# Kernel optimization log

Hardware: AMD Instinct MI355X
Metric: run time of the kernel (lower is better)

## Reference

```python
import jax, jax.numpy as jnp
import numpy as np

# Static model configuration (matches init_kwargs)
Hh, Ww = 48, 48
L = Hh * Ww            # 2304 flattened lattice sites
NH, HD = 8, 32         # heads, head_dim
D = NH * HD            # d_model = 256
MLP = 1024
NL = 4                 # num transformer blocks
RADIUS = 2             # local attention window radius
MAXD = 7               # relative position clipping
NB = 2 * MAXD + 1      # bias buckets per axis = 15
EPS = 1e-6
B = 4


def _coords():
    ys = jnp.arange(Hh)
    xs = jnp.arange(Ww)
    yy, xx = jnp.meshgrid(ys, xs, indexing='ij')
    return jnp.stack([yy, xx], axis=-1).reshape(L, 2)  # (L,2) int


def _local_mask():
    c = _coords()
    dy = jnp.abs(c[:, None, 0] - c[None, :, 0])
    dx = jnp.abs(c[:, None, 1] - c[None, :, 1])
    dy = jnp.minimum(dy, Hh - dy)  # periodic (torus)
    dx = jnp.minimum(dx, Ww - dx)
    allowed = (dy <= RADIUS) & (dx <= RADIUS)
    return jnp.where(allowed, 0.0, -1e9).astype(jnp.float32)  # (L,L)


def _rel_bias(rel_emb):
    c = _coords()
    dy = c[:, None, 0] - c[None, :, 0]
    dx = c[:, None, 1] - c[None, :, 1]
    # shortest signed periodic differences
    dy = (dy + Hh // 2) % Hh - Hh // 2
    dx = (dx + Ww // 2) % Ww - Ww // 2
    dyb = (jnp.clip(dy, -MAXD, MAXD) + MAXD).astype(jnp.int32)
    dxb = (jnp.clip(dx, -MAXD, MAXD) + MAXD).astype(jnp.int32)
    return rel_emb[:, dyb, dxb]  # (NH, L, L)


def _ln(x, s, b):
    mu = jnp.mean(x, axis=-1, keepdims=True)
    var = jnp.var(x, axis=-1, keepdims=True)
    return (x - mu) * jax.lax.rsqrt(var + EPS) * s + b


def setup_inputs() -> dict:
    key = jax.random.key(0)
    ks = jax.random.split(key, 16)
    sc = 0.05
    inp = {
        'x': jax.random.randint(ks[0], (B, Hh, Ww), 0, 2, dtype=jnp.int32),
        'Win': jax.random.normal(ks[1], (3, D), jnp.float32) * sc,
        'b_in': jnp.zeros((D,), jnp.float32),
        'lnA_s': jnp.ones((NL, D), jnp.float32),
        'lnA_b': jnp.zeros((NL, D), jnp.float32),
        'Wq': jax.random.normal(ks[2], (NL, D, NH, HD), jnp.float32) * sc,
        'bq': jnp.zeros((NL, NH, HD), jnp.float32),
        'Wk': jax.random.normal(ks[3], (NL, D, NH, HD), jnp.float32) * sc,
        'bk': jnp.zeros((NL, NH, HD), jnp.float32),
        'Wv': jax.random.normal(ks[4], (NL, D, NH, HD), jnp.float32) * sc,
        'bv': jnp.zeros((NL, NH, HD), jnp.float32),
        'Wo': jax.random.normal(ks[5], (NL, NH, HD, D), jnp.float32) * sc,
        'bo': jnp.zeros((NL, D), jnp.float32),
        'lnB_s': jnp.ones((NL, D), jnp.float32),
        'lnB_b': jnp.zeros((NL, D), jnp.float32),
        'W1': jax.random.normal(ks[6], (NL, D, MLP), jnp.float32) * sc,
        'b1': jnp.zeros((NL, MLP), jnp.float32),
        'W2': jax.random.normal(ks[7], (NL, MLP, D), jnp.float32) * sc,
        'b2': jnp.zeros((NL, D), jnp.float32),
        'rel_emb': jax.random.normal(ks[8], (NH, NB, NB), jnp.float32) * 0.02,
        'lnF_s': jnp.ones((D,), jnp.float32),
        'lnF_b': jnp.zeros((D,), jnp.float32),
        'Wout': jax.random.normal(ks[9], (D, 1), jnp.float32) * sc,
        'bout': jnp.zeros((1,), jnp.float32),
    }
    return inp


def reference(x, Win, b_in, lnA_s, lnA_b, Wq, bq, Wk, bk, Wv, bv, Wo, bo,
              lnB_s, lnB_b, W1, b1, W2, b2, rel_emb, lnF_s, lnF_b, Wout, bout):
    xf = x.astype(jnp.float32)[..., None]                     # (B,H,W,1)
    ys = jnp.arange(Hh, dtype=jnp.float32) / max(Hh - 1, 1)
    xs = jnp.arange(Ww, dtype=jnp.float32) / max(Ww - 1, 1)
    yy, xx = jnp.meshgrid(ys, xs, indexing='ij')
    coords = jnp.broadcast_to(jnp.stack([yy, xx], -1), (x.shape[0], Hh, Ww, 2))
    feats = jnp.concatenate([xf, coords], -1).reshape(x.shape[0], L, 3)

    h = feats @ Win + b_in                                    # (B,L,D)

    # combined additive attention bias: local periodic mask + learned 2D rel-pos bias
    cb = _local_mask()[None, None] + _rel_bias(rel_emb)[None]  # (1,NH,L,L)
    scale = 1.0 / np.sqrt(HD).astype(np.float32)

    for i in range(NL):
        y = _ln(h, lnA_s[i], lnA_b[i])
        q = jnp.einsum('bld,dhe->blhe', y, Wq[i]) + bq[i]
        k = jnp.einsum('bld,dhe->blhe', y, Wk[i]) + bk[i]
        v = jnp.einsum('bld,dhe->blhe', y, Wv[i]) + bv[i]
        scores = jnp.einsum('bqhe,bkhe->bhqk', q, k) * scale + cb
        p = jax.nn.softmax(scores, axis=-1)
        att = jnp.einsum('bhqk,bkhe->bqhe', p, v)
        y = jnp.einsum('bqhe,hed->bqd', att, Wo[i]) + bo[i]
        h = h + y
        y = _ln(h, lnB_s[i], lnB_b[i])
        y = jax.nn.gelu(y @ W1[i] + b1[i]) @ W2[i] + b2[i]
        h = h + y

    h = _ln(h, lnF_s, lnF_b)
    logits = (h @ Wout + bout)[..., 0].reshape(x.shape[0], Hh, Ww)
    return logits
```

## Files before the change

kernel.cpp:

```cpp
#include <hip/hip_runtime.h>
#include <hip/hip_bf16.h>
#include <math.h>

#define NT_   9216
#define D_    256
#define NH_   8
#define HD_   32
#define L_    2304
#define HH_   48
#define WW_   48
#define MLP_  1024
#define NL_   4

typedef __attribute__((ext_vector_type(8))) short bf16x8;
typedef __attribute__((ext_vector_type(4))) float f32x4;

__device__ __forceinline__ float gelu_tanh(float x) {
    const float c0 = 0.7978845608028654f;
    const float c1 = 0.044715f;
    float u = c0 * (x + c1 * x * x * x);
    return 0.5f * x * (1.0f + tanhf(u));
}

__device__ __forceinline__ void gload16(const void* gsrc, void* ldst) {
    __builtin_amdgcn_global_load_lds(
        (const __attribute__((address_space(1))) void*)gsrc,
        (__attribute__((address_space(3))) void*)ldst, 16, 0, 0);
}

__device__ __forceinline__ unsigned short f2bf(float f) {
    __hip_bfloat16 h = __float2bfloat16(f);
    return *(unsigned short*)&h;
}

__global__ void tcvt_kernel(const float* __restrict__ in, __hip_bfloat16* __restrict__ out,
                            int K, int N, int inLayerStride, int outLayerStride) {
    __shared__ float t[32][33];
    int l = blockIdx.z;
    int n0 = blockIdx.x * 32, k0 = blockIdx.y * 32;
    int tx = threadIdx.x, ty = threadIdx.y;
    const float* src = in + (size_t)l * inLayerStride;
    #pragma unroll
    for (int r = 0; r < 32; r += 8)
        t[ty + r][tx] = src[(size_t)(k0 + ty + r) * N + n0 + tx];
    __syncthreads();
    __hip_bfloat16* dst = out + (size_t)l * outLayerStride;
    #pragma unroll
    for (int r = 0; r < 32; r += 8)
        dst[(size_t)(n0 + ty + r) * K + k0 + tx] = __float2bfloat16(t[tx][ty + r]);
}

__global__ void bcat_kernel(const float* __restrict__ bq, const float* __restrict__ bk,
                            const float* __restrict__ bv, float* __restrict__ bqkv) {
    int l = blockIdx.x, n = threadIdx.x;
    float v = (n < 256) ? bq[l * 256 + n] : (n < 512 ? bk[l * 256 + n - 256] : bv[l * 256 + n - 512]);
    bqkv[l * 768 + n] = v;
}

__global__ void embed_kernel(const int* __restrict__ x, const float* __restrict__ Win,
                             const float* __restrict__ b_in, float* __restrict__ h) {
    int t = blockIdx.x, d = threadIdx.x;
    int l = t % L_;
    int yy = l / WW_, xx = l % WW_;
    float xv = (float)x[t];
    float yn = yy * (1.0f / 47.0f);
    float xn = xx * (1.0f / 47.0f);
    h[t * D_ + d] = xv * Win[d] + yn * Win[D_ + d] + xn * Win[2 * D_ + d] + b_in[d];
}

__global__ void ln_kernel(const float* __restrict__ h, const float* __restrict__ s,
                          const float* __restrict__ bb, __hip_bfloat16* __restrict__ y) {
    int wid = threadIdx.x >> 6, lane = threadIdx.x & 63;
    int t = (blockIdx.x << 2) + wid;
    float4 v = *(const float4*)(h + (size_t)t * D_ + lane * 4);
    float sum = v.x + v.y + v.z + v.w;
    float sq  = v.x * v.x + v.y * v.y + v.z * v.z + v.w * v.w;
    #pragma unroll
    for (int off = 32; off; off >>= 1) {
        sum += __shfl_xor(sum, off);
        sq  += __shfl_xor(sq,  off);
    }
    float mu  = sum * (1.0f / D_);
    float var = sq * (1.0f / D_) - mu * mu;
    float rs  = rsqrtf(var + 1e-6f);
    float4 s4 = *(const float4*)(s  + lane * 4);
    float4 b4 = *(const float4*)(bb + lane * 4);
    ushort4 o;
    o.x = f2bf((v.x - mu) * rs * s4.x + b4.x);
    o.y = f2bf((v.y - mu) * rs * s4.y + b4.y);
    o.z = f2bf((v.z - mu) * rs * s4.z + b4.z);
    o.w = f2bf((v.w - mu) * rs * s4.w + b4.w);
    *(ushort4*)(y + (size_t)t * D_ + lane * 4) = o;
}

__global__ __launch_bounds__(256)
void attn_kernel(const float* __restrict__ qkv, const float* __restrict__ rel_emb,
                 __hip_bfloat16* __restrict__ att) {
    __shared__ float ks[144 * 36];
    __shared__ float vsd[144 * 36];

    const int tile = blockIdx.x;
    const int hh   = blockIdx.y;
    const int b    = blockIdx.z;
    const int ty   = tile / 6, tx = tile - ty * 6;
    const int y0   = ty * 8,  x0  = tx * 8;
    const int tid  = threadIdx.x;

    for (int idx = tid; idx < 144 * 32; idx += 256) {
        int r = idx >> 5, d = idx & 31;
        int ly = r / 12, lx = r - ly * 12;
        int gy = y0 + ly - 2; gy += (gy < 0) ? HH_ : 0; gy -= (gy >= HH_) ? HH_ : 0;
        int gx = x0 + lx - 2; gx += (gx < 0) ? WW_ : 0; gx -= (gx >= WW_) ? WW_ : 0;
        const float* row = qkv + (size_t)(b * L_ + gy * WW_ + gx) * 768 + hh * HD_;
        ks[r * 36 + d]  = row[256 + d];
        vsd[r * 36 + d] = row[512 + d];
    }
    __syncthreads();

    const int g = tid >> 5;
    const int j = tid & 31;
    const bool valid = (j < 25);
    const int oy2 = j / 5, ox2 = j - oy2 * 5;

    const float bias = rel_emb[hh * 225 + (9 - oy2) * 15 + (9 - ox2)];

    for (int s = 0; s < 8; ++s) {
        const int t = b * L_ + (y0 + g) * WW_ + (x0 + s);

        const float* qp = qkv + (size_t)t * 768 + hh * HD_;
        const int hr = valid ? ((g + oy2) * 12 + (s + ox2)) : 0;
        const float* kp = ks + hr * 36;

        float dot = 0.f;
        #pragma unroll
        for (int d = 0; d < 8; ++d) {
            float4 q4 = ((const float4*)qp)[d];
            float4 k4 = ((const float4*)kp)[d];
            dot += q4.x * k4.x + q4.y * k4.y + q4.z * k4.z + q4.w * k4.w;
        }
        float sc = valid ? (dot * 0.17677669529663687f + bias) : -1e30f;

        float m = sc;
        #pragma unroll
        for (int off = 16; off; off >>= 1) m = fmaxf(m, __shfl_xor(m, off, 32));
        float p = __expf(sc - m);
        float sum = p;
        #pragma unroll
        for (int off = 16; off; off >>= 1) sum += __shfl_xor(sum, off, 32);
        float inv = 1.0f / sum;

        float acc = 0.f;
        #pragma unroll
        for (int n = 0; n < 25; ++n) {
            float pn = __shfl(p, n, 32);
            int   rn = (g + n / 5) * 12 + (s + n % 5);
            acc += pn * vsd[rn * 36 + j];
        }
        att[t * D_ + hh * HD_ + j] = __float2bfloat16(acc * inv);
    }
}

template<int EPI>
__global__ __launch_bounds__(256, 2)
void mgemm(const __hip_bfloat16* __restrict__ A, const __hip_bfloat16* __restrict__ BT,
           const float* __restrict__ bias, const float* res,
           float* Cf, __hip_bfloat16* Cb, int M, int N, int K) {
    __shared__ __hip_bfloat16 As[128 * 32];
    __shared__ __hip_bfloat16 Bs[128 * 32];
    const int bm = blockIdx.y * 128, bn = blockIdx.x * 128;
    const int tid = threadIdx.x, lane = tid & 63, wv = tid >> 6;
    const int wm = (wv >> 1) * 64, wn = (wv & 1) * 64;

    const __hip_bfloat16* aSrc = A + (size_t)(bm + 16 * wv + (lane >> 2)) * K + (lane & 3) * 8;
    const __hip_bfloat16* bSrc = BT + (size_t)(bn + 16 * wv + (lane >> 2)) * K + (lane & 3) * 8;
    __hip_bfloat16* aDst0 = As + wv * 512;
    __hip_bfloat16* aDst1 = As + (wv + 4) * 512;
    __hip_bfloat16* bDst0 = Bs + wv * 512;
    __hip_bfloat16* bDst1 = Bs + (wv + 4) * 512;
    const size_t rowJump = (size_t)64 * K;

    f32x4 acc[4][4];
    #pragma unroll
    for (int i = 0; i < 4; ++i)
        #pragma unroll
        for (int j = 0; j < 4; ++j)
            acc[i][j] = (f32x4){0.f, 0.f, 0.f, 0.f};

    const int rsel = (lane & 15);
    const int ko   = (lane >> 4) * 8;

    for (int k0 = 0; k0 < K; k0 += 32) {
        gload16(aSrc,            aDst0);
        gload16(aSrc + rowJump,  aDst1);
        gload16(bSrc,            bDst0);
        gload16(bSrc + rowJump,  bDst1);
        __syncthreads();

        bf16x8 af[4], bfr[4];
        #pragma unroll
        for (int f = 0; f < 4; ++f) {
            af[f]  = *(const bf16x8*)(As + (wm + f * 16 + rsel) * 32 + ko);
            bfr[f] = *(const bf16x8*)(Bs + (wn + f * 16 + rsel) * 32 + ko);
        }
        #pragma unroll
        for (int i = 0; i < 4; ++i)
            #pragma unroll
            for (int j = 0; j < 4; ++j)
                acc[i][j] = __builtin_amdgcn_mfma_f32_16x16x32_bf16(af[i], bfr[j], acc[i][j], 0, 0, 0);
        __syncthreads();
        aSrc += 32; bSrc += 32;
    }

    #pragma unroll
    for (int i = 0; i < 4; ++i) {
        #pragma unroll
        for (int r = 0; r < 4; ++r) {
            int rr = bm + wm + i * 16 + (lane >> 4) * 4 + r;
            #pragma unroll
            for (int j = 0; j < 4; ++j) {
                int cc = bn + wn + j * 16 + rsel;
                float v = acc[i][j][r] + bias[cc];
                if (EPI == 2) {
                    Cb[(size_t)rr * N + cc] = __float2bfloat16(gelu_tanh(v));
                } else {
                    if (EPI == 1) v += res[(size_t)rr * N + cc];
                    Cf[(size_t)rr * N + cc] = v;
                }
            }
        }
    }
}

__global__ void final_kernel(const float* __restrict__ h, const float* __restrict__ s,
                             const float* __restrict__ bb, const float* __restrict__ Wout,
                             const float* __restrict__ bout, float* __restrict__ out) {
    int t = blockIdx.x, d = threadIdx.x;
    float v = h[t * D_ + d];
    float a = v, b2 = v * v;
    #pragma unroll
    for (int off = 32; off; off >>= 1) {
        a  += __shfl_xor(a,  off);
        b2 += __shfl_xor(b2, off);
    }
    __shared__ float red[8];
    __shared__ float red2[4];
    int wave = threadIdx.x >> 6;
    if ((threadIdx.x & 63) == 0) { red[wave] = a; red[4 + wave] = b2; }
    __syncthreads();
    float sum   = red[0] + red[1] + red[2] + red[3];
    float sumsq = red[4] + red[5] + red[6] + red[7];
    float mu  = sum * (1.0f / D_);
    float var = sumsq * (1.0f / D_) - mu * mu;
    float rs  = rsqrtf(var + 1e-6f);
    float yv  = (v - mu) * rs * s[d] + bb[d];
    float p   = yv * Wout[d];
    #pragma unroll
    for (int off = 32; off; off >>= 1) p += __shfl_xor(p, off);
    if ((threadIdx.x & 63) == 0) red2[wave] = p;
    __syncthreads();
    if (threadIdx.x == 0)
        out[t] = red2[0] + red2[1] + red2[2] + red2[3] + bout[0];
}

extern "C" void kernel_launch(void* const* d_in, const int* in_sizes, int n_in,
                              void* d_out, int out_size, void* d_ws, size_t ws_size,
                              hipStream_t stream) {
    const int*   x       = (const int*)  d_in[0];
    const float* Win     = (const float*)d_in[1];
    const float* b_in    = (const float*)d_in[2];
    const float* lnA_s   = (const float*)d_in[3];
    const float* lnA_b   = (const float*)d_in[4];
    const float* Wq      = (const float*)d_in[5];
    const float* bq      = (const float*)d_in[6];
    const float* Wk      = (const float*)d_in[7];
    const float* bk      = (const float*)d_in[8];
    const float* Wv      = (const float*)d_in[9];
    const float* bv      = (const float*)d_in[10];
    const float* Wo      = (const float*)d_in[11];
    const float* bo      = (const float*)d_in[12];
    const float* lnB_s   = (const float*)d_in[13];
    const float* lnB_b   = (const float*)d_in[14];
    const float* W1      = (const float*)d_in[15];
    const float* b1      = (const float*)d_in[16];
    const float* W2      = (const float*)d_in[17];
    const float* b2      = (const float*)d_in[18];
    const float* rel_emb = (const float*)d_in[19];
    const float* lnF_s   = (const float*)d_in[20];
    const float* lnF_b   = (const float*)d_in[21];
    const float* Wout    = (const float*)d_in[22];
    const float* bout    = (const float*)d_in[23];
    float* out = (float*)d_out;

    float* ws = (float*)d_ws;
    float*          h      = ws;
    __hip_bfloat16* y      = (__hip_bfloat16*)(ws + 2359296);
    float*          qkv    = ws + 3538944;
    __hip_bfloat16* att    = (__hip_bfloat16*)(ws + 10616832);
    __hip_bfloat16* tbuf   = (__hip_bfloat16*)qkv;
    __hip_bfloat16* WqkvT  = (__hip_bfloat16*)(ws + 11796480);
    __hip_bfloat16* WoT    = WqkvT + 4 * 768 * 256;
    __hip_bfloat16* W1T    = WoT   + 4 * 256 * 256;
    __hip_bfloat16* W2T    = W1T   + 4 * 1024 * 256;
    float*          bqkv   = (float*)(W2T + 4 * 256 * 1024);

    dim3 blk(256);
    dim3 tb(32, 8);

    tcvt_kernel<<<dim3(8, 8, 4),  tb, 0, stream>>>(Wq, WqkvT,              256, 256,  65536, 196608);
    tcvt_kernel<<<dim3(8, 8, 4),  tb, 0, stream>>>(Wk, WqkvT + 256 * 256,  256, 256,  65536, 196608);
    tcvt_kernel<<<dim3(8, 8, 4),  tb, 0, stream>>>(Wv, WqkvT + 512 * 256,  256, 256,  65536, 196608);
    tcvt_kernel<<<dim3(8, 8, 4),  tb, 0, stream>>>(Wo, WoT,                256, 256,  65536, 65536);
    tcvt_kernel<<<dim3(32, 8, 4), tb, 0, stream>>>(W1, W1T,                256, 1024, 262144, 262144);
    tcvt_kernel<<<dim3(8, 32, 4), tb, 0, stream>>>(W2, W2T,                1024, 256, 262144, 262144);
    bcat_kernel<<<4, 768, 0, stream>>>(bq, bk, bv, bqkv);

    embed_kernel<<<NT_, blk, 0, stream>>>(x, Win, b_in, h);

    for (int l = 0; l < NL_; ++l) {
        const __hip_bfloat16* wqkv = WqkvT + (size_t)l * 768 * 256;
        const __hip_bfloat16* wo   = WoT   + (size_t)l * 256 * 256;
        const __hip_bfloat16* w1   = W1T   + (size_t)l * 1024 * 256;
        const __hip_bfloat16* w2   = W2T   + (size_t)l * 256 * 1024;

        ln_kernel<<<NT_ / 4, blk, 0, stream>>>(h, lnA_s + l * D_, lnA_b + l * D_, y);

        mgemm<0><<<dim3(6, 72), blk, 0, stream>>>(y, wqkv, bqkv + l * 768, nullptr,
                                                  qkv, nullptr, NT_, 768, 256);
        attn_kernel<<<dim3(36, 8, 4), blk, 0, stream>>>(qkv, rel_emb, att);
        mgemm<1><<<dim3(2, 72), blk, 0, stream>>>(att, wo, bo + l * D_, h,
                                                  h, nullptr, NT_, 256, 256);

        ln_kernel<<<NT_ / 4, blk, 0, stream>>>(h, lnB_s + l * D_, lnB_b + l * D_, y);

        mgemm<2><<<dim3(8, 72), blk, 0, stream>>>(y, w1, b1 + l * MLP_, nullptr,
                                                  nullptr, tbuf, NT_, 1024, 256);
        mgemm<1><<<dim3(2, 72), blk, 0, stream>>>(tbuf, w2, b2 + l * D_, h,
                                                  h, nullptr, NT_, 256, 1024);
    }

    final_kernel<<<NT_, blk, 0, stream>>>(h, lnF_s, lnF_b, Wout, bout, out);
}
```

Before: 666.0 us.

## Fuse weight prep launches, vectorize attention K/V loads, remap GEMM tiles per XCD

Merges the six weight transpose/convert launches and the bias concat into a single prep kernel, removing several kernel launches. The attention kernel now stages K/V halo rows into shared memory with float4 loads instead of scalar loads. The GEMM remaps its linear block index so consecutive tiles are grouped per XCD (stride by 8), aiming for better L2 locality on the multi-die chip. The remap assumes the block count is divisible by 8.

```diff
diff --git a/kernel.cpp b/kernel.cpp
--- a/kernel.cpp
+++ b/kernel.cpp
@@ -33,28 +33,56 @@
     return *(unsigned short*)&h;
 }
 
-__global__ void tcvt_kernel(const float* __restrict__ in, __hip_bfloat16* __restrict__ out,
-                            int K, int N, int inLayerStride, int outLayerStride) {
+__global__ void prep_kernel(const float* __restrict__ Wq, const float* __restrict__ Wk,
+                            const float* __restrict__ Wv, const float* __restrict__ Wo,
+                            const float* __restrict__ W1, const float* __restrict__ W2,
+                            const float* __restrict__ bq, const float* __restrict__ bk,
+                            const float* __restrict__ bv,
+                            __hip_bfloat16* __restrict__ WqkvT, __hip_bfloat16* __restrict__ WoT,
+                            __hip_bfloat16* __restrict__ W1T, __hip_bfloat16* __restrict__ W2T,
+                            float* __restrict__ bqkv) {
+    int bid = blockIdx.x;
+    int tid = threadIdx.y * 32 + threadIdx.x;
+    if (bid >= 3072) {
+        int l = bid - 3072;
+        for (int n = tid; n < 768; n += 256) {
+            float v = (n < 256) ? bq[l * 256 + n]
+                    : (n < 512 ? bk[l * 256 + n - 256] : bv[l * 256 + n - 512]);
+            bqkv[l * 768 + n] = v;
+        }
+        return;
+    }
+    int l = bid / 768, rem = bid - l * 768;
+    const float* src; __hip_bfloat16* dst;
+    int K, N, n0, k0;
+    if (rem < 256) {
+        int which = rem >> 6, tidx = rem & 63;
+        n0 = (tidx & 7) * 32; k0 = (tidx >> 3) * 32;
+        K = 256; N = 256;
+        if (which == 0)      { src = Wq + (size_t)l * 65536; dst = WqkvT + (size_t)l * 196608; }
+        else if (which == 1) { src = Wk + (size_t)l * 65536; dst = WqkvT + (size_t)l * 196608 + 65536; }
+        else if (which == 2) { src = Wv + (size_t)l * 65536; dst = WqkvT + (size_t)l * 196608 + 131072; }
+        else                 { src = Wo + (size_t)l * 65536; dst = WoT   + (size_t)l * 65536; }
+    } else if (rem < 512) {
+        int tidx = rem - 256;
+        n0 = (tidx & 31) * 32; k0 = (tidx >> 5) * 32;
+        K = 256; N = 1024;
+        src = W1 + (size_t)l * 262144; dst = W1T + (size_t)l * 262144;
+    } else {
+        int tidx = rem - 512;
+        n0 = (tidx & 7) * 32; k0 = (tidx >> 3) * 32;
+        K = 1024; N = 256;
+        src = W2 + (size_t)l * 262144; dst = W2T + (size_t)l * 262144;
+    }
     __shared__ float t[32][33];
-    int l = blockIdx.z;
-    int n0 = blockIdx.x * 32, k0 = blockIdx.y * 32;
     int tx = threadIdx.x, ty = threadIdx.y;
-    const float* src = in + (size_t)l * inLayerStride;
     #pragma unroll
     for (int r = 0; r < 32; r += 8)
         t[ty + r][tx] = src[(size_t)(k0 + ty + r) * N + n0 + tx];
     __syncthreads();
-    __hip_bfloat16* dst = out + (size_t)l * outLayerStride;
     #pragma unroll
     for (int r = 0; r < 32; r += 8)
         dst[(size_t)(n0 + ty + r) * K + k0 + tx] = __float2bfloat16(t[tx][ty + r]);
-}
-
-__global__ void bcat_kernel(const float* __restrict__ bq, const float* __restrict__ bk,
-                            const float* __restrict__ bv, float* __restrict__ bqkv) {
-    int l = blockIdx.x, n = threadIdx.x;
-    float v = (n < 256) ? bq[l * 256 + n] : (n < 512 ? bk[l * 256 + n - 256] : bv[l * 256 + n - 512]);
-    bqkv[l * 768 + n] = v;
 }
 
 __global__ void embed_kernel(const int* __restrict__ x, const float* __restrict__ Win,
@@ -106,14 +134,14 @@
     const int y0   = ty * 8,  x0  = tx * 8;
     const int tid  = threadIdx.x;
 
-    for (int idx = tid; idx < 144 * 32; idx += 256) {
-        int r = idx >> 5, d = idx & 31;
+    for (int idx = tid; idx < 144 * 8; idx += 256) {
+        int r = idx >> 3, c = (idx & 7) * 4;
         int ly = r / 12, lx = r - ly * 12;
         int gy = y0 + ly - 2; gy += (gy < 0) ? HH_ : 0; gy -= (gy >= HH_) ? HH_ : 0;
         int gx = x0 + lx - 2; gx += (gx < 0) ? WW_ : 0; gx -= (gx >= WW_) ? WW_ : 0;
-        const float* row = qkv + (size_t)(b * L_ + gy * WW_ + gx) * 768 + hh * HD_;
-        ks[r * 36 + d]  = row[256 + d];
-        vsd[r * 36 + d] = row[512 + d];
+        const float* row = qkv + (size_t)(b * L_ + gy * WW_ + gx) * 768 + hh * HD_ + c;
+        *(float4*)(ks  + r * 36 + c) = *(const float4*)(row + 256);
+        *(float4*)(vsd + r * 36 + c) = *(const float4*)(row + 512);
     }
     __syncthreads();
 
@@ -167,7 +195,14 @@
            float* Cf, __hip_bfloat16* Cb, int M, int N, int K) {
     __shared__ __hip_bfloat16 As[128 * 32];
     __shared__ __hip_bfloat16 Bs[128 * 32];
-    const int bm = blockIdx.y * 128, bn = blockIdx.x * 128;
+
+    const int nwg = gridDim.x * gridDim.y;
+    const int cpx = nwg >> 3;
+    const int lin = blockIdx.y * gridDim.x + blockIdx.x;
+    const int tile = (lin & 7) * cpx + (lin >> 3);
+    const int bm = (tile / gridDim.x) * 128;
+    const int bn = (tile % gridDim.x) * 128;
+
     const int tid = threadIdx.x, lane = tid & 63, wv = tid >> 6;
     const int wm = (wv >> 1) * 64, wn = (wv & 1) * 64;
 
@@ -304,15 +339,10 @@
     float*          bqkv   = (float*)(W2T + 4 * 256 * 1024);
 
     dim3 blk(256);
-    dim3 tb(32, 8);
-
-    tcvt_kernel<<<dim3(8, 8, 4),  tb, 0, stream>>>(Wq, WqkvT,              256, 256,  65536, 196608);
-    tcvt_kernel<<<dim3(8, 8, 4),  tb, 0, stream>>>(Wk, WqkvT + 256 * 256,  256, 256,  65536, 196608);
-    tcvt_kernel<<<dim3(8, 8, 4),  tb, 0, stream>>>(Wv, WqkvT + 512 * 256,  256, 256,  65536, 196608);
-    tcvt_kernel<<<dim3(8, 8, 4),  tb, 0, stream>>>(Wo, WoT,                256, 256,  65536, 65536);
-    tcvt_kernel<<<dim3(32, 8, 4), tb, 0, stream>>>(W1, W1T,                256, 1024, 262144, 262144);
-    tcvt_kernel<<<dim3(8, 32, 4), tb, 0, stream>>>(W2, W2T,                1024, 256, 262144, 262144);
-    bcat_kernel<<<4, 768, 0, stream>>>(bq, bk, bv, bqkv);
+
+    prep_kernel<<<3076, dim3(32, 8), 0, stream>>>(Wq, Wk, Wv, Wo, W1, W2,
+                                                  bq, bk, bv,
+                                                  WqkvT, WoT, W1T, W2T, bqkv);
 
     embed_kernel<<<NT_, blk, 0, stream>>>(x, Win, b_in, h);
 
```

After: 631.9 us. 1.05x faster.
